# Optimization experiments

Measured on AMD Instinct MI355X. Metric: run time of the kernel, lower is better.

Reference implementation:

```python
import jax, jax.numpy as jnp
import numpy as np

T, H, I, E, TOP_K = 1024, 1024, 512, 16, 4
SHARED_I = 512  # moe_intermediate_size * n_shared_experts


def setup_inputs() -> dict:
    key = jax.random.key(0)
    ks = jax.random.split(key, 6)
    s = 0.02
    return {
        "hidden_states": jax.random.normal(ks[0], (T, H), dtype=jnp.float32),
        "gate_w": jax.random.normal(ks[1], (E, H), dtype=jnp.float32) * s,          # router weight
        "w_gate_up": jax.random.normal(ks[2], (E, H, 2 * I), dtype=jnp.float32) * s,  # per-expert merged gate/up
        "w_down": jax.random.normal(ks[3], (E, I, H), dtype=jnp.float32) * s,
        "shared_gate_up": jax.random.normal(ks[4], (H, 2 * SHARED_I), dtype=jnp.float32) * s,
        "shared_down": jax.random.normal(ks[5], (SHARED_I, H), dtype=jnp.float32) * s,
    }


def _swiglu(gu):
    g, u = jnp.split(gu, 2, axis=-1)  # gate first, then up (SiluAndMul)
    return jax.nn.silu(g) * u


def reference(hidden_states, gate_w, w_gate_up, w_down, shared_gate_up, shared_down):
    x = hidden_states  # [T, H]
    # ---- router: sigmoid scoring, plain top-k (num_expert_group=topk_group=1), renormalize ----
    logits = x @ gate_w.T                      # [T, E]
    scores = jax.nn.sigmoid(logits)            # [T, E]
    topk_vals, topk_idx = jax.lax.top_k(scores, TOP_K)
    topk_w = topk_vals / jnp.sum(topk_vals, axis=-1, keepdims=True)
    # dense routing matrix [T, E] (zeros for unselected experts)
    route = jnp.zeros_like(scores).at[jnp.arange(T)[:, None], topk_idx].set(topk_w)
    # ---- routed experts: grouped SwiGLU GEMMs, combined by routing weights ----
    gu = jnp.einsum('th,ehf->etf', x, w_gate_up)   # [E, T, 2I]
    h = _swiglu(gu)                                 # [E, T, I]
    eo = jnp.einsum('eti,eih->eth', h, w_down)      # [E, T, H]
    routed = jnp.einsum('te,eth->th', route, eo)    # [T, H]
    # ---- shared expert (routed_scaling_factor = 1.0) ----
    shared = _swiglu(x @ shared_gate_up) @ shared_down  # [T, H]
    return routed + shared
```

## Files before the change

kernel.cpp:

```cpp
#include <hip/hip_runtime.h>
#include <hip/hip_bf16.h>
#include <cstdint>

#define T_TOK 1024
#define H_DIM 1024
#define I_DIM 512
#define E_NUM 16
#define TOPK  4

typedef __bf16 bf16;
typedef __bf16 bf16x8 __attribute__((ext_vector_type(8)));
typedef float  f32x4  __attribute__((ext_vector_type(4)));

#define GLOAD16(g, l)                                                                   \
  __builtin_amdgcn_global_load_lds((const __attribute__((address_space(1))) void*)(g),  \
                                   (__attribute__((address_space(3))) void*)(l), 16, 0, 0)


__device__ __forceinline__ void transpose_tile(const float* __restrict__ src,
                                               bf16* __restrict__ dst, int K, int N,
                                               int kb, int nb, int tid, bf16* tile) {
  {
    const int k = tid >> 2, nq = (tid & 3) * 16;
    const float4* s = (const float4*)(src + (size_t)(kb + k) * N + nb + nq);
    float4 f[4];
#pragma unroll
    for (int q = 0; q < 4; ++q) f[q] = s[q];
    const float* fs = (const float*)f;
#pragma unroll
    for (int j = 0; j < 16; ++j) tile[(nq + j) * 72 + k] = (bf16)fs[j];
  }
  __syncthreads();
  {
    const int n = tid >> 2, kq = (tid & 3) * 16;
    bf16x8 p0 = *(const bf16x8*)(tile + n * 72 + kq);
    bf16x8 p1 = *(const bf16x8*)(tile + n * 72 + kq + 8);
    bf16* d = dst + (size_t)(nb + n) * K + kb + kq;
    *(bf16x8*)d = p0;
    *(bf16x8*)(d + 8) = p1;
  }
}

__global__ void prep_kernel(const float* __restrict__ x, bf16* __restrict__ xb,
                            const float* __restrict__ wgu, bf16* __restrict__ wguT,
                            const float* __restrict__ sgu, bf16* __restrict__ sguT,
                            const float* __restrict__ wd, bf16* __restrict__ wdT,
                            const float* __restrict__ sd, bf16* __restrict__ sdT,
                            const float* __restrict__ gw,
                            int* __restrict__ topk_e, float* __restrict__ topk_w,
                            int* __restrict__ counts, int* __restrict__ tok,
                            float* __restrict__ wt, int* __restrict__ slot) {
  __shared__ __align__(16) bf16 tile[64 * 72];
  const int b = blockIdx.x, tid = threadIdx.x;

  if (b < 4352) {
    const int z = b >> 8, r = b & 255;
    const float* src = (z < E_NUM) ? (wgu + (size_t)z * H_DIM * 2 * I_DIM) : sgu;
    bf16*       dst  = (z < E_NUM) ? (wguT + (size_t)z * H_DIM * 2 * I_DIM) : sguT;
    transpose_tile(src, dst, H_DIM, 2 * I_DIM, (r >> 4) * 64, (r & 15) * 64, tid, tile);
  } else if (b < 6528) {
    const int i = b - 4352, z = i >> 7, r = i & 127;
    const float* src = (z < E_NUM) ? (wd + (size_t)z * I_DIM * H_DIM) : sd;
    bf16*       dst  = (z < E_NUM) ? (wdT + (size_t)z * I_DIM * H_DIM) : sdT;
    transpose_tile(src, dst, I_DIM, H_DIM, (r >> 4) * 64, (r & 15) * 64, tid, tile);
  } else if (b < 7040) {
    const int i = (b - 6528) * 256 + tid;
    float4 f0 = ((const float4*)x)[i * 2];
    float4 f1 = ((const float4*)x)[i * 2 + 1];
    bf16x8 p;
    p[0]=(bf16)f0.x; p[1]=(bf16)f0.y; p[2]=(bf16)f0.z; p[3]=(bf16)f0.w;
    p[4]=(bf16)f1.x; p[5]=(bf16)f1.y; p[6]=(bf16)f1.z; p[7]=(bf16)f1.w;
    ((bf16x8*)xb)[i] = p;
  } else if (b < 7296) {
    const int wave = tid >> 6, lane = tid & 63;
    const int t = (b - 7040) * 4 + wave;
    const float4* xr = (const float4*)(x + (size_t)t * H_DIM);
    float4 xv[4];
#pragma unroll
    for (int j = 0; j < 4; ++j) xv[j] = xr[lane + 64 * j];
    float p[E_NUM];
#pragma unroll
    for (int e = 0; e < E_NUM; ++e) {
      const float4* gr = (const float4*)(gw + (size_t)e * H_DIM);
      float s = 0.f;
#pragma unroll
      for (int j = 0; j < 4; ++j) {
        float4 g = gr[lane + 64 * j];
        s += xv[j].x * g.x + xv[j].y * g.y + xv[j].z * g.z + xv[j].w * g.w;
      }
      p[e] = s;
    }
#pragma unroll
    for (int off = 32; off > 0; off >>= 1) {
#pragma unroll
      for (int e = 0; e < E_NUM; ++e) p[e] += __shfl_xor(p[e], off);
    }
    float rem[E_NUM];
#pragma unroll
    for (int e = 0; e < E_NUM; ++e) rem[e] = 1.f / (1.f + __expf(-p[e]));
    float vals[TOPK]; int idx[TOPK];
#pragma unroll
    for (int k = 0; k < TOPK; ++k) {
      float m = rem[0]; int mi = 0;
#pragma unroll
      for (int e = 1; e < E_NUM; ++e) {
        if (rem[e] > m) { m = rem[e]; mi = e; }
      }
      vals[k] = m; idx[k] = mi;
#pragma unroll
      for (int e = 0; e < E_NUM; ++e) rem[e] = (e == mi) ? -1e30f : rem[e];
    }
    if (lane == 0) {
      float inv = 1.f / (vals[0] + vals[1] + vals[2] + vals[3]);
      int4 ids; ids.x = idx[0]; ids.y = idx[1]; ids.z = idx[2]; ids.w = idx[3];
      float4 w4; w4.x = vals[0]*inv; w4.y = vals[1]*inv; w4.z = vals[2]*inv; w4.w = vals[3]*inv;
      ((int4*)topk_e)[t] = ids;
      ((float4*)topk_w)[t] = w4;
    }
  } else {
    const int i = (b - 7296) * 256 + tid;
    if (i == 0) counts[E_NUM] = T_TOK;
    tok [E_NUM * T_TOK + i] = i;
    wt  [E_NUM * T_TOK + i] = 1.0f;
    slot[E_NUM * T_TOK + i] = T_TOK * TOPK + i;
  }
}

__global__ void router_build_kernel(const int* __restrict__ topk_e, const float* __restrict__ topk_w,
                                    int* __restrict__ counts, int* __restrict__ tok,
                                    float* __restrict__ wt, int* __restrict__ slot) {
  const int e = blockIdx.x;
  const int tid = threadIdx.x, wave = tid >> 6, lane = tid & 63;
  __shared__ int wsum[4];
  int base = 0;
  for (int r = 0; r < 4; ++r) {
    int t = r * 256 + tid;
    int4 ids = ((const int4*)topk_e)[t];
    int match = -1;
    if (ids.x == e) match = 0;
    if (ids.y == e) match = 1;
    if (ids.z == e) match = 2;
    if (ids.w == e) match = 3;
    unsigned long long bm = __ballot(match >= 0);
    int prefix = __popcll(bm & ((1ull << lane) - 1ull));
    if (lane == 0) wsum[wave] = __popcll(bm);
    __syncthreads();
    int wbase = 0;
#pragma unroll
    for (int wv = 0; wv < 4; ++wv) wbase += (wv < wave) ? wsum[wv] : 0;
    int total = wsum[0] + wsum[1] + wsum[2] + wsum[3];
    if (match >= 0) {
      int pos = base + wbase + prefix;
      tok [e * T_TOK + pos] = t;
      wt  [e * T_TOK + pos] = topk_w[t * 4 + match];
      slot[e * T_TOK + pos] = t * 4 + match;
    }
    base += total;
    __syncthreads();
  }
  if (tid == 0) counts[e] = base;
}

__global__ __launch_bounds__(256, 4)
void gemm1_kernel(const bf16* __restrict__ xb, const bf16* __restrict__ wguT,
                  const bf16* __restrict__ sguT, const int* __restrict__ counts,
                  const int* __restrict__ tok, const float* __restrict__ wt,
                  const int* __restrict__ slot, bf16* __restrict__ hbuf) {
  const int e   = blockIdx.z;
  const int cnt = counts[e];
  const int rt  = blockIdx.y;
  if (rt * 64 >= cnt) return;
  const int nb = blockIdx.x * 64;
  const bf16* BT = (e < E_NUM) ? (wguT + (size_t)e * (2 * I_DIM) * H_DIM) : sguT;

  __shared__ __align__(16) bf16 sA[3][64 * 32];
  __shared__ __align__(16) bf16 sG[3][64 * 32];
  __shared__ __align__(16) bf16 sU[3][64 * 32];

  const int tid = threadIdx.x, wave = tid >> 6, lane = tid & 63;
  const int wr = wave >> 1, wc = wave & 1;
  const int fr = lane & 15, kg = lane >> 4;
  const int lr = lane >> 2, lk = (lane & 3) * 8;

  int ar = rt * 64 + wave * 16 + lr;
  int arc = ar < cnt ? ar : cnt - 1;
  const bf16* aS = xb + (size_t)tok[e * T_TOK + arc] * H_DIM + lk;
  const bf16* gS = BT + (size_t)(nb + wave * 16 + lr) * H_DIM + lk;
  const bf16* uS = BT + (size_t)(I_DIM + nb + wave * 16 + lr) * H_DIM + lk;
  const int ldsOff = wave * 512;

  f32x4 accg[2][2], accu[2][2];
#pragma unroll
  for (int i = 0; i < 2; ++i)
#pragma unroll
    for (int j = 0; j < 2; ++j) { accg[i][j] = f32x4{0,0,0,0}; accu[i][j] = f32x4{0,0,0,0}; }

#define STG1(t, bidx) do { int ko = (t) * 32;   \
    GLOAD16(aS + ko, sA[bidx] + ldsOff);        \
    GLOAD16(gS + ko, sG[bidx] + ldsOff);        \
    GLOAD16(uS + ko, sU[bidx] + ldsOff); } while (0)

  STG1(0, 0); STG1(1, 1);
  const int NT = H_DIM / 32;
  int bufc = 0;
  for (int t = 0; t < NT; ++t) {
    int bn = bufc + 2; bn = bn >= 3 ? bn - 3 : bn;
    if (t + 2 < NT) {
      STG1(t + 2, bn);
      asm volatile("s_waitcnt vmcnt(6)" ::: "memory");
    } else if (t + 1 < NT) {
      asm volatile("s_waitcnt vmcnt(3)" ::: "memory");
    } else {
      asm volatile("s_waitcnt vmcnt(0)" ::: "memory");
    }
    __builtin_amdgcn_s_barrier();
    __builtin_amdgcn_sched_barrier(0);
    const bf16* A = sA[bufc];
    const bf16* G = sG[bufc];
    const bf16* U = sU[bufc];
    bf16x8 a0 = *(const bf16x8*)(A + (wr * 32      + fr) * 32 + kg * 8);
    bf16x8 a1 = *(const bf16x8*)(A + (wr * 32 + 16 + fr) * 32 + kg * 8);
    bf16x8 g0 = *(const bf16x8*)(G + (wc * 32      + fr) * 32 + kg * 8);
    bf16x8 g1 = *(const bf16x8*)(G + (wc * 32 + 16 + fr) * 32 + kg * 8);
    bf16x8 u0 = *(const bf16x8*)(U + (wc * 32      + fr) * 32 + kg * 8);
    bf16x8 u1 = *(const bf16x8*)(U + (wc * 32 + 16 + fr) * 32 + kg * 8);
    accg[0][0] = __builtin_amdgcn_mfma_f32_16x16x32_bf16(a0, g0, accg[0][0], 0, 0, 0);
    accg[0][1] = __builtin_amdgcn_mfma_f32_16x16x32_bf16(a0, g1, accg[0][1], 0, 0, 0);
    accg[1][0] = __builtin_amdgcn_mfma_f32_16x16x32_bf16(a1, g0, accg[1][0], 0, 0, 0);
    accg[1][1] = __builtin_amdgcn_mfma_f32_16x16x32_bf16(a1, g1, accg[1][1], 0, 0, 0);
    accu[0][0] = __builtin_amdgcn_mfma_f32_16x16x32_bf16(a0, u0, accu[0][0], 0, 0, 0);
    accu[0][1] = __builtin_amdgcn_mfma_f32_16x16x32_bf16(a0, u1, accu[0][1], 0, 0, 0);
    accu[1][0] = __builtin_amdgcn_mfma_f32_16x16x32_bf16(a1, u0, accu[1][0], 0, 0, 0);
    accu[1][1] = __builtin_amdgcn_mfma_f32_16x16x32_bf16(a1, u1, accu[1][1], 0, 0, 0);
    __builtin_amdgcn_sched_barrier(0);
    __builtin_amdgcn_s_barrier();
    bufc = bufc == 2 ? 0 : bufc + 1;
  }
#undef STG1

#pragma unroll
  for (int mi = 0; mi < 2; ++mi) {
#pragma unroll
    for (int j = 0; j < 4; ++j) {
      int grow = rt * 64 + wr * 32 + mi * 16 + kg * 4 + j;
      if (grow < cnt) {
        bf16* hr = hbuf + (size_t)slot[e * T_TOK + grow] * I_DIM;
        float w = wt[e * T_TOK + grow];
#pragma unroll
        for (int ni = 0; ni < 2; ++ni) {
          float g = accg[mi][ni][j], u = accu[mi][ni][j];
          float h = w * (g / (1.f + __expf(-g))) * u;
          hr[nb + wc * 32 + ni * 16 + fr] = (bf16)h;
        }
      }
    }
  }
}

__global__ __launch_bounds__(256, 4)
void gemm2_kernel(const bf16* __restrict__ hbuf, const bf16* __restrict__ wdT,
                  const bf16* __restrict__ sdT, const int* __restrict__ counts,
                  const int* __restrict__ slot, float* __restrict__ obuf) {
  const int e   = blockIdx.z;
  const int cnt = counts[e];
  const int rt  = blockIdx.y;
  if (rt * 64 >= cnt) return;
  const int nb = blockIdx.x * 128;
  const bf16* BT = (e < E_NUM) ? (wdT + (size_t)e * H_DIM * I_DIM) : sdT;

  __shared__ __align__(16) bf16 sA[3][64 * 32];
  __shared__ __align__(16) bf16 sB[3][128 * 32];

  const int tid = threadIdx.x, wave = tid >> 6, lane = tid & 63;
  const int wr = wave >> 1, wc = wave & 1;
  const int fr = lane & 15, kg = lane >> 4;
  const int lr = lane >> 2, lk = (lane & 3) * 8;

  int ar = rt * 64 + wave * 16 + lr;
  int arc = ar < cnt ? ar : cnt - 1;
  const bf16* aS  = hbuf + (size_t)slot[e * T_TOK + arc] * I_DIM + lk;
  const bf16* bS0 = BT + (size_t)(nb + wave * 32 + lr) * I_DIM + lk;
  const bf16* bS1 = bS0 + (size_t)16 * I_DIM;
  const int aOff  = wave * 512;
  const int bOff0 = wave * 1024;
  const int bOff1 = bOff0 + 512;

  f32x4 acc[2][4];
#pragma unroll
  for (int i = 0; i < 2; ++i)
#pragma unroll
    for (int j = 0; j < 4; ++j) acc[i][j] = f32x4{0,0,0,0};

#define STG2(t, bidx) do { int ko = (t) * 32;   \
    GLOAD16(aS  + ko, sA[bidx] + aOff);         \
    GLOAD16(bS0 + ko, sB[bidx] + bOff0);        \
    GLOAD16(bS1 + ko, sB[bidx] + bOff1); } while (0)

  STG2(0, 0); STG2(1, 1);
  const int NT = I_DIM / 32;
  int bufc = 0;
  for (int t = 0; t < NT; ++t) {
    int bn = bufc + 2; bn = bn >= 3 ? bn - 3 : bn;
    if (t + 2 < NT) {
      STG2(t + 2, bn);
      asm volatile("s_waitcnt vmcnt(6)" ::: "memory");
    } else if (t + 1 < NT) {
      asm volatile("s_waitcnt vmcnt(3)" ::: "memory");
    } else {
      asm volatile("s_waitcnt vmcnt(0)" ::: "memory");
    }
    __builtin_amdgcn_s_barrier();
    __builtin_amdgcn_sched_barrier(0);
    const bf16* A = sA[bufc];
    const bf16* B = sB[bufc];
    bf16x8 a0 = *(const bf16x8*)(A + (wr * 32      + fr) * 32 + kg * 8);
    bf16x8 a1 = *(const bf16x8*)(A + (wr * 32 + 16 + fr) * 32 + kg * 8);
    bf16x8 b[4];
#pragma unroll
    for (int ni = 0; ni < 4; ++ni)
      b[ni] = *(const bf16x8*)(B + (wc * 64 + ni * 16 + fr) * 32 + kg * 8);
#pragma unroll
    for (int ni = 0; ni < 4; ++ni) {
      acc[0][ni] = __builtin_amdgcn_mfma_f32_16x16x32_bf16(a0, b[ni], acc[0][ni], 0, 0, 0);
      acc[1][ni] = __builtin_amdgcn_mfma_f32_16x16x32_bf16(a1, b[ni], acc[1][ni], 0, 0, 0);
    }
    __builtin_amdgcn_sched_barrier(0);
    __builtin_amdgcn_s_barrier();
    bufc = bufc == 2 ? 0 : bufc + 1;
  }
#undef STG2

#pragma unroll
  for (int mi = 0; mi < 2; ++mi) {
#pragma unroll
    for (int j = 0; j < 4; ++j) {
      int grow = rt * 64 + wr * 32 + mi * 16 + kg * 4 + j;
      if (grow < cnt) {
        float* orow = obuf + (size_t)slot[e * T_TOK + grow] * H_DIM + nb + wc * 64 + fr;
#pragma unroll
        for (int ni = 0; ni < 4; ++ni)
          orow[ni * 16] = acc[mi][ni][j];
      }
    }
  }
}

__global__ void reduce_kernel(const float* __restrict__ obuf, float* __restrict__ out) {
  const int t = blockIdx.x;
  const int c = threadIdx.x;
  const f32x4* o4 = (const f32x4*)obuf;
  f32x4 s = o4[(size_t)(t * 4 + 0) * 256 + c];
  s += o4[(size_t)(t * 4 + 1) * 256 + c];
  s += o4[(size_t)(t * 4 + 2) * 256 + c];
  s += o4[(size_t)(t * 4 + 3) * 256 + c];
  s += o4[(size_t)(T_TOK * TOPK + t) * 256 + c];
  ((f32x4*)out)[(size_t)t * 256 + c] = s;
}

extern "C" void kernel_launch(void* const* d_in, const int* in_sizes, int n_in,
                              void* d_out, int out_size, void* d_ws, size_t ws_size,
                              hipStream_t stream) {
  const float* x   = (const float*)d_in[0];
  const float* gw  = (const float*)d_in[1];
  const float* wgu = (const float*)d_in[2];
  const float* wd  = (const float*)d_in[3];
  const float* sgu = (const float*)d_in[4];
  const float* sd  = (const float*)d_in[5];
  float* out = (float*)d_out;

  char* ws = (char*)d_ws;
  int*   counts = (int*)  (ws);
  int*   tok    = (int*)  (ws + 1024);
  float* wtA    = (float*)(ws + 70656);
  int*   slotA  = (int*)  (ws + 140288);
  int*   topk_e = (int*)  (ws + 209920);
  float* topk_w = (float*)(ws + 226304);
  bf16*  xb     = (bf16*) (ws + 245760);
  bf16*  hbuf   = (bf16*) (ws + 2342912);
  bf16*  wguT   = (bf16*) (ws + 7585792);
  bf16*  wdT    = (bf16*) (ws + 41140224);
  bf16*  sguT   = (bf16*) (ws + 57917440);
  bf16*  sdT    = (bf16*) (ws + 60014592);
  float* obuf   = (float*)(ws + 7585792);

  prep_kernel<<<7300, 256, 0, stream>>>(x, xb, wgu, wguT, sgu, sguT, wd, wdT, sd, sdT,
                                        gw, topk_e, topk_w, counts, tok, wtA, slotA);
  router_build_kernel<<<E_NUM, 256, 0, stream>>>(topk_e, topk_w, counts, tok, wtA, slotA);
  gemm1_kernel<<<dim3(8, 16, 17), 256, 0, stream>>>(xb, wguT, sguT, counts, tok, wtA, slotA, hbuf);
  gemm2_kernel<<<dim3(8, 16, 17), 256, 0, stream>>>(hbuf, wdT, sdT, counts, slotA, obuf);
  reduce_kernel<<<T_TOK, 256, 0, stream>>>(obuf, out);
}
```

Baseline: 96.53 us.

## Drop weight transpose in prep; read row-major weights via LDS transpose loads

The prep kernel no longer transposes expert weights through an LDS tile. It now does a straight elementwise fp32-to-bf16 conversion that keeps the original [K,N] layout. Both GEMM kernels stage row-major weight tiles and build MFMA B operands with ds_read_b64_tr_b16 transpose reads. This removes the shared-memory transpose and barrier from the bandwidth-bound prep pass. In exchange it adds explicit lgkmcnt waits and relies on a specific lane-to-address mapping for the transposed LDS reads.

```diff
diff --git a/kernel.cpp b/kernel.cpp
--- a/kernel.cpp
+++ b/kernel.cpp
@@ -9,6 +9,7 @@
 #define TOPK  4
 
 typedef __bf16 bf16;
+typedef __bf16 bf16x4 __attribute__((ext_vector_type(4)));
 typedef __bf16 bf16x8 __attribute__((ext_vector_type(8)));
 typedef float  f32x4  __attribute__((ext_vector_type(4)));
 
@@ -16,64 +17,54 @@
   __builtin_amdgcn_global_load_lds((const __attribute__((address_space(1))) void*)(g),  \
                                    (__attribute__((address_space(3))) void*)(l), 16, 0, 0)
 
-
-__device__ __forceinline__ void transpose_tile(const float* __restrict__ src,
-                                               bf16* __restrict__ dst, int K, int N,
-                                               int kb, int nb, int tid, bf16* tile) {
-  {
-    const int k = tid >> 2, nq = (tid & 3) * 16;
-    const float4* s = (const float4*)(src + (size_t)(kb + k) * N + nb + nq);
-    float4 f[4];
-#pragma unroll
-    for (int q = 0; q < 4; ++q) f[q] = s[q];
-    const float* fs = (const float*)f;
-#pragma unroll
-    for (int j = 0; j < 16; ++j) tile[(nq + j) * 72 + k] = (bf16)fs[j];
-  }
-  __syncthreads();
-  {
-    const int n = tid >> 2, kq = (tid & 3) * 16;
-    bf16x8 p0 = *(const bf16x8*)(tile + n * 72 + kq);
-    bf16x8 p1 = *(const bf16x8*)(tile + n * 72 + kq + 8);
-    bf16* d = dst + (size_t)(nb + n) * K + kb + kq;
-    *(bf16x8*)d = p0;
-    *(bf16x8*)(d + 8) = p1;
-  }
+__device__ __forceinline__ unsigned lds_addr(const bf16* p) {
+  return (unsigned)(uintptr_t)(const __attribute__((address_space(3))) bf16*)p;
+}
+
+template <int OFF>
+__device__ __forceinline__ bf16x4 tr_read(unsigned addr) {
+  bf16x4 r;
+  if constexpr (OFF == 0)
+    asm volatile("ds_read_b64_tr_b16 %0, %1" : "=v"(r) : "v"(addr));
+  else if constexpr (OFF == 512)
+    asm volatile("ds_read_b64_tr_b16 %0, %1 offset:512" : "=v"(r) : "v"(addr));
+  else
+    asm volatile("ds_read_b64_tr_b16 %0, %1 offset:1024" : "=v"(r) : "v"(addr));
+  return r;
+}
+
+__device__ __forceinline__ bf16x8 cat8(bf16x4 a, bf16x4 b) {
+  return __builtin_shufflevector(a, b, 0, 1, 2, 3, 4, 5, 6, 7);
+}
+
+__device__ __forceinline__ void conv8(const float* __restrict__ src, bf16* __restrict__ dst,
+                                      int i) {
+  float4 f0 = ((const float4*)src)[i * 2];
+  float4 f1 = ((const float4*)src)[i * 2 + 1];
+  bf16x8 p;
+  p[0]=(bf16)f0.x; p[1]=(bf16)f0.y; p[2]=(bf16)f0.z; p[3]=(bf16)f0.w;
+  p[4]=(bf16)f1.x; p[5]=(bf16)f1.y; p[6]=(bf16)f1.z; p[7]=(bf16)f1.w;
+  ((bf16x8*)dst)[i] = p;
 }
 
 __global__ void prep_kernel(const float* __restrict__ x, bf16* __restrict__ xb,
-                            const float* __restrict__ wgu, bf16* __restrict__ wguT,
-                            const float* __restrict__ sgu, bf16* __restrict__ sguT,
-                            const float* __restrict__ wd, bf16* __restrict__ wdT,
-                            const float* __restrict__ sd, bf16* __restrict__ sdT,
+                            const float* __restrict__ wgu, bf16* __restrict__ wguB,
+                            const float* __restrict__ wd, bf16* __restrict__ wdB,
+                            const float* __restrict__ sgu, bf16* __restrict__ sguB,
+                            const float* __restrict__ sd, bf16* __restrict__ sdB,
                             const float* __restrict__ gw,
                             int* __restrict__ topk_e, float* __restrict__ topk_w,
                             int* __restrict__ counts, int* __restrict__ tok,
                             float* __restrict__ wt, int* __restrict__ slot) {
-  __shared__ __align__(16) bf16 tile[64 * 72];
   const int b = blockIdx.x, tid = threadIdx.x;
-
-  if (b < 4352) {
-    const int z = b >> 8, r = b & 255;
-    const float* src = (z < E_NUM) ? (wgu + (size_t)z * H_DIM * 2 * I_DIM) : sgu;
-    bf16*       dst  = (z < E_NUM) ? (wguT + (size_t)z * H_DIM * 2 * I_DIM) : sguT;
-    transpose_tile(src, dst, H_DIM, 2 * I_DIM, (r >> 4) * 64, (r & 15) * 64, tid, tile);
-  } else if (b < 6528) {
-    const int i = b - 4352, z = i >> 7, r = i & 127;
-    const float* src = (z < E_NUM) ? (wd + (size_t)z * I_DIM * H_DIM) : sd;
-    bf16*       dst  = (z < E_NUM) ? (wdT + (size_t)z * I_DIM * H_DIM) : sdT;
-    transpose_tile(src, dst, I_DIM, H_DIM, (r >> 4) * 64, (r & 15) * 64, tid, tile);
-  } else if (b < 7040) {
-    const int i = (b - 6528) * 256 + tid;
-    float4 f0 = ((const float4*)x)[i * 2];
-    float4 f1 = ((const float4*)x)[i * 2 + 1];
-    bf16x8 p;
-    p[0]=(bf16)f0.x; p[1]=(bf16)f0.y; p[2]=(bf16)f0.z; p[3]=(bf16)f0.w;
-    p[4]=(bf16)f1.x; p[5]=(bf16)f1.y; p[6]=(bf16)f1.z; p[7]=(bf16)f1.w;
-    ((bf16x8*)xb)[i] = p;
-  } else if (b < 7296) {
+  if (b < 8192)        conv8(wgu, wguB, b * 256 + tid);
+  else if (b < 12288)  conv8(wd, wdB, (b - 8192) * 256 + tid);
+  else if (b < 12800)  conv8(sgu, sguB, (b - 12288) * 256 + tid);
+  else if (b < 13056)  conv8(sd, sdB, (b - 12800) * 256 + tid);
+  else if (b < 13568)  conv8(x, xb, (b - 13056) * 256 + tid);
+  else if (b < 13824) {
     const int wave = tid >> 6, lane = tid & 63;
-    const int t = (b - 7040) * 4 + wave;
+    const int t = (b - 13568) * 4 + wave;
     const float4* xr = (const float4*)(x + (size_t)t * H_DIM);
     float4 xv[4];
 #pragma unroll
@@ -118,7 +109,7 @@
       ((float4*)topk_w)[t] = w4;
     }
   } else {
-    const int i = (b - 7296) * 256 + tid;
+    const int i = (b - 13824) * 256 + tid;
     if (i == 0) counts[E_NUM] = T_TOK;
     tok [E_NUM * T_TOK + i] = i;
     wt  [E_NUM * T_TOK + i] = 1.0f;
@@ -162,8 +153,8 @@
 }
 
 __global__ __launch_bounds__(256, 4)
-void gemm1_kernel(const bf16* __restrict__ xb, const bf16* __restrict__ wguT,
-                  const bf16* __restrict__ sguT, const int* __restrict__ counts,
+void gemm1_kernel(const bf16* __restrict__ xb, const bf16* __restrict__ wguB,
+                  const bf16* __restrict__ sguB, const int* __restrict__ counts,
                   const int* __restrict__ tok, const float* __restrict__ wt,
                   const int* __restrict__ slot, bf16* __restrict__ hbuf) {
   const int e   = blockIdx.z;
@@ -171,11 +162,11 @@
   const int rt  = blockIdx.y;
   if (rt * 64 >= cnt) return;
   const int nb = blockIdx.x * 64;
-  const bf16* BT = (e < E_NUM) ? (wguT + (size_t)e * (2 * I_DIM) * H_DIM) : sguT;
+  const bf16* WB = (e < E_NUM) ? (wguB + (size_t)e * H_DIM * (2 * I_DIM)) : sguB;
 
   __shared__ __align__(16) bf16 sA[3][64 * 32];
-  __shared__ __align__(16) bf16 sG[3][64 * 32];
-  __shared__ __align__(16) bf16 sU[3][64 * 32];
+  __shared__ __align__(16) bf16 sG[3][2048];
+  __shared__ __align__(16) bf16 sU[3][2048];
 
   const int tid = threadIdx.x, wave = tid >> 6, lane = tid & 63;
   const int wr = wave >> 1, wc = wave & 1;
@@ -185,9 +176,13 @@
   int ar = rt * 64 + wave * 16 + lr;
   int arc = ar < cnt ? ar : cnt - 1;
   const bf16* aS = xb + (size_t)tok[e * T_TOK + arc] * H_DIM + lk;
-  const bf16* gS = BT + (size_t)(nb + wave * 16 + lr) * H_DIM + lk;
-  const bf16* uS = BT + (size_t)(I_DIM + nb + wave * 16 + lr) * H_DIM + lk;
-  const int ldsOff = wave * 512;
+  const int aOff = wave * 512;
+
+  const int k_off = 8 * wave + 4 * (lane >> 5) + ((lane & 7) >> 1);
+  const int n_off = 16 * ((lane >> 3) & 3) + 8 * (lane & 1);
+  const bf16* gS = WB + (size_t)k_off * (2 * I_DIM) + nb + n_off;
+  const bf16* uS = WB + (size_t)k_off * (2 * I_DIM) + I_DIM + nb + n_off;
+  const int wOff = wave * 512;
 
   f32x4 accg[2][2], accu[2][2];
 #pragma unroll
@@ -195,10 +190,10 @@
 #pragma unroll
     for (int j = 0; j < 2; ++j) { accg[i][j] = f32x4{0,0,0,0}; accu[i][j] = f32x4{0,0,0,0}; }
 
-#define STG1(t, bidx) do { int ko = (t) * 32;   \
-    GLOAD16(aS + ko, sA[bidx] + ldsOff);        \
-    GLOAD16(gS + ko, sG[bidx] + ldsOff);        \
-    GLOAD16(uS + ko, sU[bidx] + ldsOff); } while (0)
+#define STG1(t, bidx) do { size_t ko = (size_t)(t) * 32;    \
+    GLOAD16(aS + ko, sA[bidx] + aOff);                      \
+    GLOAD16(gS + ko * (2 * I_DIM), sG[bidx] + wOff);        \
+    GLOAD16(uS + ko * (2 * I_DIM), sU[bidx] + wOff); } while (0)
 
   STG1(0, 0); STG1(1, 1);
   const int NT = H_DIM / 32;
@@ -216,14 +211,17 @@
     __builtin_amdgcn_s_barrier();
     __builtin_amdgcn_sched_barrier(0);
     const bf16* A = sA[bufc];
-    const bf16* G = sG[bufc];
-    const bf16* U = sU[bufc];
     bf16x8 a0 = *(const bf16x8*)(A + (wr * 32      + fr) * 32 + kg * 8);
     bf16x8 a1 = *(const bf16x8*)(A + (wr * 32 + 16 + fr) * 32 + kg * 8);
-    bf16x8 g0 = *(const bf16x8*)(G + (wc * 32      + fr) * 32 + kg * 8);
-    bf16x8 g1 = *(const bf16x8*)(G + (wc * 32 + 16 + fr) * 32 + kg * 8);
-    bf16x8 u0 = *(const bf16x8*)(U + (wc * 32      + fr) * 32 + kg * 8);
-    bf16x8 u1 = *(const bf16x8*)(U + (wc * 32 + 16 + fr) * 32 + kg * 8);
+    unsigned gb = lds_addr(sG[bufc]) + (unsigned)((lane >> 4) << 10) + (unsigned)((lane & 15) << 3);
+    unsigned ub = lds_addr(sU[bufc]) + (unsigned)((lane >> 4) << 10) + (unsigned)((lane & 15) << 3);
+    unsigned nb0 = (unsigned)(wc * 256), nb1 = nb0 + 128;
+    bf16x8 g0 = cat8(tr_read<0>(gb + nb0), tr_read<512>(gb + nb0));
+    bf16x8 g1 = cat8(tr_read<0>(gb + nb1), tr_read<512>(gb + nb1));
+    bf16x8 u0 = cat8(tr_read<0>(ub + nb0), tr_read<512>(ub + nb0));
+    bf16x8 u1 = cat8(tr_read<0>(ub + nb1), tr_read<512>(ub + nb1));
+    asm volatile("s_waitcnt lgkmcnt(0)" ::: "memory");
+    __builtin_amdgcn_sched_barrier(0);
     accg[0][0] = __builtin_amdgcn_mfma_f32_16x16x32_bf16(a0, g0, accg[0][0], 0, 0, 0);
     accg[0][1] = __builtin_amdgcn_mfma_f32_16x16x32_bf16(a0, g1, accg[0][1], 0, 0, 0);
     accg[1][0] = __builtin_amdgcn_mfma_f32_16x16x32_bf16(a1, g0, accg[1][0], 0, 0, 0);
@@ -258,18 +256,18 @@
 }
 
 __global__ __launch_bounds__(256, 4)
-void gemm2_kernel(const bf16* __restrict__ hbuf, const bf16* __restrict__ wdT,
-                  const bf16* __restrict__ sdT, const int* __restrict__ counts,
+void gemm2_kernel(const bf16* __restrict__ hbuf, const bf16* __restrict__ wdB,
+                  const bf16* __restrict__ sdB, const int* __restrict__ counts,
                   const int* __restrict__ slot, float* __restrict__ obuf) {
   const int e   = blockIdx.z;
   const int cnt = counts[e];
   const int rt  = blockIdx.y;
   if (rt * 64 >= cnt) return;
   const int nb = blockIdx.x * 128;
-  const bf16* BT = (e < E_NUM) ? (wdT + (size_t)e * H_DIM * I_DIM) : sdT;
+  const bf16* WB = (e < E_NUM) ? (wdB + (size_t)e * I_DIM * H_DIM) : sdB;
 
   __shared__ __align__(16) bf16 sA[3][64 * 32];
-  __shared__ __align__(16) bf16 sB[3][128 * 32];
+  __shared__ __align__(16) bf16 sB[3][4096];
 
   const int tid = threadIdx.x, wave = tid >> 6, lane = tid & 63;
   const int wr = wave >> 1, wc = wave & 1;
@@ -278,10 +276,13 @@
 
   int ar = rt * 64 + wave * 16 + lr;
   int arc = ar < cnt ? ar : cnt - 1;
-  const bf16* aS  = hbuf + (size_t)slot[e * T_TOK + arc] * I_DIM + lk;
-  const bf16* bS0 = BT + (size_t)(nb + wave * 32 + lr) * I_DIM + lk;
-  const bf16* bS1 = bS0 + (size_t)16 * I_DIM;
-  const int aOff  = wave * 512;
+  const bf16* aS = hbuf + (size_t)slot[e * T_TOK + arc] * I_DIM + lk;
+  const int aOff = wave * 512;
+
+  const int j2 = (lane & 7) >> 1, h2 = lane & 1, nblk2 = lane >> 3;
+  const int n2 = nb + nblk2 * 16 + 8 * h2;
+  const bf16* bS0 = WB + (size_t)((wave * 2 + 0) * 4 + j2) * H_DIM + n2;
+  const bf16* bS1 = WB + (size_t)((wave * 2 + 1) * 4 + j2) * H_DIM + n2;
   const int bOff0 = wave * 1024;
   const int bOff1 = bOff0 + 512;
 
@@ -291,10 +292,10 @@
 #pragma unroll
     for (int j = 0; j < 4; ++j) acc[i][j] = f32x4{0,0,0,0};
 
-#define STG2(t, bidx) do { int ko = (t) * 32;   \
-    GLOAD16(aS  + ko, sA[bidx] + aOff);         \
-    GLOAD16(bS0 + ko, sB[bidx] + bOff0);        \
-    GLOAD16(bS1 + ko, sB[bidx] + bOff1); } while (0)
+#define STG2(t, bidx) do { size_t ko = (size_t)(t) * 32;    \
+    GLOAD16(aS + ko, sA[bidx] + aOff);                      \
+    GLOAD16(bS0 + ko * H_DIM, sB[bidx] + bOff0);            \
+    GLOAD16(bS1 + ko * H_DIM, sB[bidx] + bOff1); } while (0)
 
   STG2(0, 0); STG2(1, 1);
   const int NT = I_DIM / 32;
@@ -312,13 +313,16 @@
     __builtin_amdgcn_s_barrier();
     __builtin_amdgcn_sched_barrier(0);
     const bf16* A = sA[bufc];
-    const bf16* B = sB[bufc];
     bf16x8 a0 = *(const bf16x8*)(A + (wr * 32      + fr) * 32 + kg * 8);
     bf16x8 a1 = *(const bf16x8*)(A + (wr * 32 + 16 + fr) * 32 + kg * 8);
+    unsigned bb = lds_addr(sB[bufc]) + (unsigned)((lane >> 4) << 11) + (unsigned)((lane & 15) << 3)
+                + (unsigned)(wc * 512);
     bf16x8 b[4];
 #pragma unroll
     for (int ni = 0; ni < 4; ++ni)
-      b[ni] = *(const bf16x8*)(B + (wc * 64 + ni * 16 + fr) * 32 + kg * 8);
+      b[ni] = cat8(tr_read<0>(bb + ni * 128), tr_read<1024>(bb + ni * 128));
+    asm volatile("s_waitcnt lgkmcnt(0)" ::: "memory");
+    __builtin_amdgcn_sched_barrier(0);
 #pragma unroll
     for (int ni = 0; ni < 4; ++ni) {
       acc[0][ni] = __builtin_amdgcn_mfma_f32_16x16x32_bf16(a0, b[ni], acc[0][ni], 0, 0, 0);
@@ -377,16 +381,16 @@
   float* topk_w = (float*)(ws + 226304);
   bf16*  xb     = (bf16*) (ws + 245760);
   bf16*  hbuf   = (bf16*) (ws + 2342912);
-  bf16*  wguT   = (bf16*) (ws + 7585792);
-  bf16*  wdT    = (bf16*) (ws + 41140224);
-  bf16*  sguT   = (bf16*) (ws + 57917440);
-  bf16*  sdT    = (bf16*) (ws + 60014592);
+  bf16*  wguB   = (bf16*) (ws + 7585792);
+  bf16*  wdB    = (bf16*) (ws + 41140224);
+  bf16*  sguB   = (bf16*) (ws + 57917440);
+  bf16*  sdB    = (bf16*) (ws + 60014592);
   float* obuf   = (float*)(ws + 7585792);
 
-  prep_kernel<<<7300, 256, 0, stream>>>(x, xb, wgu, wguT, sgu, sguT, wd, wdT, sd, sdT,
-                                        gw, topk_e, topk_w, counts, tok, wtA, slotA);
+  prep_kernel<<<13828, 256, 0, stream>>>(x, xb, wgu, wguB, wd, wdB, sgu, sguB, sd, sdB,
+                                         gw, topk_e, topk_w, counts, tok, wtA, slotA);
   router_build_kernel<<<E_NUM, 256, 0, stream>>>(topk_e, topk_w, counts, tok, wtA, slotA);
-  gemm1_kernel<<<dim3(8, 16, 17), 256, 0, stream>>>(xb, wguT, sguT, counts, tok, wtA, slotA, hbuf);
-  gemm2_kernel<<<dim3(8, 16, 17), 256, 0, stream>>>(hbuf, wdT, sdT, counts, slotA, obuf);
+  gemm1_kernel<<<dim3(8, 16, 17), 256, 0, stream>>>(xb, wguB, sguB, counts, tok, wtA, slotA, hbuf);
+  gemm2_kernel<<<dim3(8, 16, 17), 256, 0, stream>>>(hbuf, wdB, sdB, counts, slotA, obuf);
   reduce_kernel<<<T_TOK, 256, 0, stream>>>(obuf, out);
 }
```

After: 97.44 us. No clear change (+0.9%).
